# Optimization experiments

Measured on AMD Instinct MI355X. Metric: run time of the kernel, lower is better.

Reference implementation:

```python
import jax, jax.numpy as jnp
import numpy as np

B, N, D_IN, D_OUT = 512, 64, 2048, 1024
EPS = 1e-12  # layer_norm_epsilon


def setup_inputs() -> dict:
    key = jax.random.key(0)
    k0, k1, k2, k3, k4 = jax.random.split(key, 5)
    img_feats = jax.random.normal(k0, (B, N, D_IN), jnp.float32)
    boxes = jax.random.normal(k1, (B, N, 7), jnp.float32)
    box_mask = jax.random.randint(k2, (B, N), 0, 2, jnp.int32)
    obj_labels = jax.random.randint(k3, (B, N), 0, 91, jnp.int32)
    # Learned params: obj_downsample Linear(2048->1024), LayerNorm(1024)
    W = jax.random.normal(k4, (D_IN, D_OUT), jnp.float32) * 0.02
    b = jnp.zeros((D_OUT,), jnp.float32)
    ln_w = jnp.ones((D_OUT,), jnp.float32)
    ln_b = jnp.zeros((D_OUT,), jnp.float32)
    return {"img_feats": img_feats, "boxes": boxes, "box_mask": box_mask,
            "obj_labels": obj_labels, "W": W, "b": b, "ln_w": ln_w, "ln_b": ln_b}


def reference(img_feats, boxes, box_mask, obj_labels, W, b, ln_w, ln_b):
    # Dropout(p=0.1) is identity in eval mode.
    # Linear + ReLU applied to every (padded) box; per-row ops so padded rows
    # are computed then masked — same math as gathering valid rows first.
    h = jax.nn.relu(jnp.einsum('bnd,df->bnf', img_feats, W) + b)  # [B,N,1024]
    mu = jnp.mean(h, axis=-1, keepdims=True)
    var = jnp.mean(jnp.square(h - mu), axis=-1, keepdims=True)
    ln = (h - mu) * jax.lax.rsqrt(var + EPS) * ln_w + ln_b  # LayerNorm
    # pad_sequence repack: left-align each image's valid boxes (stable sort
    # keeps original order among valid boxes), zero the padded tail.
    order = jnp.argsort(1 - box_mask, axis=1, stable=True)  # valid first
    packed = jnp.take_along_axis(ln, order[:, :, None], axis=1)
    m = jnp.take_along_axis(box_mask, order, axis=1).astype(ln.dtype)
    return packed * m[:, :, None]  # obj_reps: [B, N, 1024]
```

## Files before the change

### kernel.cpp

```cpp
#include <hip/hip_runtime.h>
#include <hip/hip_bf16.h>

typedef __attribute__((ext_vector_type(8))) short short8;
typedef __attribute__((ext_vector_type(4))) short short4v;
typedef __attribute__((ext_vector_type(4))) float f32x4;

#define D_IN   2048
#define D_OUT  1024

__device__ __forceinline__ short f2bf(float x) {
    union { __hip_bfloat16 h; short s; } u;
    u.h = __float2bfloat16(x);
    return u.s;
}

__global__ void transpose_w_kernel(const float* __restrict__ W,
                                   short* __restrict__ Bt) {
    __shared__ float tile[32][33];
    int c0 = blockIdx.x * 32;
    int r0 = blockIdx.y * 32;
    int tc = threadIdx.x & 31;
    int tr = threadIdx.x >> 5;
#pragma unroll
    for (int i = 0; i < 32; i += 8)
        tile[tr + i][tc] = W[(long)(r0 + tr + i) * D_OUT + c0 + tc];
    __syncthreads();
#pragma unroll
    for (int i = 0; i < 32; i += 8)
        Bt[(long)(c0 + tr + i) * D_IN + r0 + tc] = f2bf(tile[tc][tr + i]);
}


#define BAR()    __builtin_amdgcn_s_barrier()
#define SB0()    __builtin_amdgcn_sched_barrier(0)
#define LGKM0()  do { asm volatile("s_waitcnt lgkmcnt(0)" ::: "memory"); SB0(); } while (0)

__global__ __launch_bounds__(512, 2)
void fused_kernel(const float* __restrict__ img, const short* __restrict__ Bt,
                  const float* __restrict__ bias, const int* __restrict__ mask,
                  const float* __restrict__ lnw, const float* __restrict__ lnb,
                  float* __restrict__ out) {
    __shared__ char LDS[69632];

    const int b    = blockIdx.x;
    const int tid  = threadIdx.x;
    const int lane = tid & 63;
    const int w    = tid >> 6;
    const int lrow = lane & 15;
    const int lchk = lane >> 4;

    const int brow = tid >> 2;
    const int bchk = tid & 3;
    const int bswz = bchk ^ (brow & 3) ^ ((tid >> 4) & 3);
    const short* bsrc = Bt + (long)brow * D_IN + bchk * 8;
    char* bdst = LDS + brow * 64 + bswz * 16;
    const int arl   = tid >> 3;
    const long arowg = (long)b * 64 + arl;
    const int ak4   = (tid & 7) * 4;
    const int achk  = (tid & 7) >> 1;
    char* adst = LDS + 65536 + arl * 64
               + ((achk ^ (arl & 3) ^ ((arl >> 2) & 3)) * 16) + (tid & 1) * 8;
    const int fsw = ((lchk ^ (lrow & 3) ^ ((lrow >> 2) & 3)) << 4);
    const char* afb = LDS + 65536 + lrow * 64 + fsw;
    const char* bfb = LDS + w * 8192 + lrow * 64 + fsw;

    f32x4 acc[4][8];
#pragma unroll
    for (int i = 0; i < 4; ++i)
#pragma unroll
        for (int j = 0; j < 8; ++j) acc[i][j] = (f32x4)0.0f;

    short8 bst[8];
    float4 stA;
    short8 fa[4], fb[8];

    stA = *(const float4*)(img + arowg * D_IN + ak4);
#pragma unroll
    for (int j = 0; j < 8; ++j)
        bst[j] = *(const short8*)(bsrc + (long)j * 128 * D_IN);

#pragma unroll 1
    for (int t = 0; t < 64; ++t) {
        BAR(); SB0();
        {
            short4v ca;
            ca[0] = f2bf(stA.x); ca[1] = f2bf(stA.y);
            ca[2] = f2bf(stA.z); ca[3] = f2bf(stA.w);
            *(short4v*)adst = ca;
        }
#pragma unroll
        for (int j = 0; j < 8; ++j)
            *(short8*)(bdst + j * 8192) = bst[j];
        {
            int k1 = ((t + 1) & 63) * 32;
            stA = *(const float4*)(img + arowg * D_IN + k1 + ak4);
#pragma unroll
            for (int j = 0; j < 8; ++j)
                bst[j] = *(const short8*)(bsrc + (long)j * 128 * D_IN + k1);
        }
        LGKM0();
        BAR(); SB0();
#pragma unroll
        for (int mi = 0; mi < 4; ++mi)
            fa[mi] = *(const short8*)(afb + mi * 1024);
#pragma unroll
        for (int nf = 0; nf < 8; ++nf)
            fb[nf] = *(const short8*)(bfb + nf * 1024);
        __builtin_amdgcn_s_setprio(1);
#pragma unroll
        for (int mi = 0; mi < 4; ++mi)
#pragma unroll
            for (int nf = 0; nf < 8; ++nf)
                acc[mi][nf] = __builtin_amdgcn_mfma_f32_16x16x32_bf16(
                    fa[mi], fb[nf], acc[mi][nf], 0, 0, 0);
        __builtin_amdgcn_s_setprio(0);
    }

    __syncthreads();

    float* redS = (float*)LDS;
    float* redQ = (float*)(LDS + 2048);
    float* muT  = (float*)(LDS + 4096);
    float* rsT  = (float*)(LDS + 4352);

    float bb[8];
#pragma unroll
    for (int nf = 0; nf < 8; ++nf) bb[nf] = bias[w * 128 + nf * 16 + lrow];

    float s[4][4], q[4][4];
#pragma unroll
    for (int mi = 0; mi < 4; ++mi)
#pragma unroll
        for (int r = 0; r < 4; ++r) { s[mi][r] = 0.f; q[mi][r] = 0.f; }
#pragma unroll
    for (int mi = 0; mi < 4; ++mi)
#pragma unroll
        for (int nf = 0; nf < 8; ++nf)
#pragma unroll
            for (int r = 0; r < 4; ++r) {
                float v = fmaxf(acc[mi][nf][r] + bb[nf], 0.f);
                acc[mi][nf][r] = v;
                s[mi][r] += v;
                q[mi][r] += v * v;
            }
#pragma unroll
    for (int mi = 0; mi < 4; ++mi)
#pragma unroll
        for (int r = 0; r < 4; ++r)
#pragma unroll
            for (int off = 1; off <= 8; off <<= 1) {
                s[mi][r] += __shfl_xor(s[mi][r], off);
                q[mi][r] += __shfl_xor(q[mi][r], off);
            }
    if (lrow == 0) {
#pragma unroll
        for (int mi = 0; mi < 4; ++mi)
#pragma unroll
            for (int r = 0; r < 4; ++r) {
                int m = mi * 16 + lchk * 4 + r;
                redS[w * 64 + m] = s[mi][r];
                redQ[w * 64 + m] = q[mi][r];
            }
    }
    __syncthreads();
    if (tid < 64) {
        float S = 0.f, Q = 0.f;
#pragma unroll
        for (int ww = 0; ww < 8; ++ww) { S += redS[ww * 64 + tid]; Q += redQ[ww * 64 + tid]; }
        float mu  = S * (1.0f / 1024.0f);
        float var = Q * (1.0f / 1024.0f) - mu * mu;
        muT[tid] = mu;
        rsT[tid] = rsqrtf(var + 1e-12f);
    }
    __syncthreads();

    int mv = mask[(b << 6) | lane];
    unsigned long long bal = __ballot(mv != 0);
    int cnt = __popcll(bal);

    float lw[8], lb[8];
#pragma unroll
    for (int nf = 0; nf < 8; ++nf) {
        int col = w * 128 + nf * 16 + lrow;
        lw[nf] = lnw[col];
        lb[nf] = lnb[col];
    }
#pragma unroll
    for (int mi = 0; mi < 4; ++mi)
#pragma unroll
        for (int r = 0; r < 4; ++r) {
            int m = mi * 16 + lchk * 4 + r;
            if ((bal >> m) & 1ull) {
                int d = __popcll(bal & ((1ull << m) - 1ull));
                float mu = muT[m], rs = rsT[m];
                long obase = ((long)(b << 6) + d) * D_OUT + w * 128 + lrow;
#pragma unroll
                for (int nf = 0; nf < 8; ++nf)
                    out[obase + nf * 16] = (acc[mi][nf][r] - mu) * rs * lw[nf] + lb[nf];
            }
        }
    for (int d = cnt; d < 64; ++d) {
        float2 z = make_float2(0.f, 0.f);
        *(float2*)(out + ((long)(b << 6) + d) * D_OUT + w * 128 + lane * 2) = z;
    }
}

extern "C" void kernel_launch(void* const* d_in, const int* in_sizes, int n_in,
                              void* d_out, int out_size, void* d_ws, size_t ws_size,
                              hipStream_t stream) {
    const float* img  = (const float*)d_in[0];
    const int*   mask = (const int*)d_in[2];
    const float* W    = (const float*)d_in[4];
    const float* bias = (const float*)d_in[5];
    const float* lnw  = (const float*)d_in[6];
    const float* lnb  = (const float*)d_in[7];
    float* out = (float*)d_out;

    short* Bt = (short*)d_ws;

    transpose_w_kernel<<<dim3(D_OUT / 32, D_IN / 32), 256, 0, stream>>>(W, Bt);
    fused_kernel<<<512, 512, 0, stream>>>(img, Bt, bias, mask, lnw, lnb, out);
}
```

Measured before the change: 281.3 us.

## Load B fragments directly from global into registers, bypassing LDS staging

The weight tile is no longer staged through shared memory. Each wave loads its MFMA B fragments straight from the transposed bf16 weight buffer into registers, double-buffered across two k-steps with the loop unrolled by two. LDS shrinks to 8 KB for the A tile only. This removes the B LDS writes, the B LDS reads and much of the LDS footprint. In exchange, every wave issues uncached-pattern global loads per k-step and relies on L2 for reuse, and register pressure rises from the extra fragment buffer.

```diff
diff --git a/kernel.cpp b/kernel.cpp
--- a/kernel.cpp
+++ b/kernel.cpp
@@ -40,7 +40,7 @@
                   const float* __restrict__ bias, const int* __restrict__ mask,
                   const float* __restrict__ lnw, const float* __restrict__ lnb,
                   float* __restrict__ out) {
-    __shared__ char LDS[69632];
+    __shared__ char LDS[8192];
 
     const int b    = blockIdx.x;
     const int tid  = threadIdx.x;
@@ -49,20 +49,16 @@
     const int lrow = lane & 15;
     const int lchk = lane >> 4;
 
-    const int brow = tid >> 2;
-    const int bchk = tid & 3;
-    const int bswz = bchk ^ (brow & 3) ^ ((tid >> 4) & 3);
-    const short* bsrc = Bt + (long)brow * D_IN + bchk * 8;
-    char* bdst = LDS + brow * 64 + bswz * 16;
     const int arl   = tid >> 3;
     const long arowg = (long)b * 64 + arl;
     const int ak4   = (tid & 7) * 4;
     const int achk  = (tid & 7) >> 1;
-    char* adst = LDS + 65536 + arl * 64
+    char* adst = LDS + arl * 64
                + ((achk ^ (arl & 3) ^ ((arl >> 2) & 3)) * 16) + (tid & 1) * 8;
     const int fsw = ((lchk ^ (lrow & 3) ^ ((lrow >> 2) & 3)) << 4);
-    const char* afb = LDS + 65536 + lrow * 64 + fsw;
-    const char* bfb = LDS + w * 8192 + lrow * 64 + fsw;
+    const char* afb = LDS + lrow * 64 + fsw;
+
+    const short* bsrc = Bt + (long)(w * 128 + lrow) * D_IN + lchk * 8;
 
     f32x4 acc[4][8];
 #pragma unroll
@@ -70,50 +66,55 @@
 #pragma unroll
         for (int j = 0; j < 8; ++j) acc[i][j] = (f32x4)0.0f;
 
-    short8 bst[8];
     float4 stA;
-    short8 fa[4], fb[8];
+    short8 bA[8], bB[8], fa[4];
+
+#define A_WRITE() do {                                                          \
+    short4v ca;                                                                 \
+    ca[0] = f2bf(stA.x); ca[1] = f2bf(stA.y);                                   \
+    ca[2] = f2bf(stA.z); ca[3] = f2bf(stA.w);                                   \
+    *(short4v*)adst = ca;                                                       \
+} while (0)
+#define FA_READ() do {                                                          \
+    _Pragma("unroll") for (int mi = 0; mi < 4; ++mi)                            \
+        fa[mi] = *(const short8*)(afb + mi * 1024);                             \
+} while (0)
+#define B_LOAD(dst, kt) do {                                                    \
+    _Pragma("unroll") for (int nf = 0; nf < 8; ++nf)                            \
+        dst[nf] = *(const short8*)(bsrc + (long)nf * 16 * D_IN + (kt) * 32);    \
+} while (0)
+#define MFMA_T(fb) do {                                                         \
+    __builtin_amdgcn_s_setprio(1);                                              \
+    _Pragma("unroll") for (int mi = 0; mi < 4; ++mi)                            \
+    _Pragma("unroll") for (int nf = 0; nf < 8; ++nf)                            \
+        acc[mi][nf] = __builtin_amdgcn_mfma_f32_16x16x32_bf16(                  \
+            fa[mi], fb[nf], acc[mi][nf], 0, 0, 0);                              \
+    __builtin_amdgcn_s_setprio(0);                                              \
+} while (0)
 
     stA = *(const float4*)(img + arowg * D_IN + ak4);
-#pragma unroll
-    for (int j = 0; j < 8; ++j)
-        bst[j] = *(const short8*)(bsrc + (long)j * 128 * D_IN);
+    B_LOAD(bA, 0);
 
 #pragma unroll 1
-    for (int t = 0; t < 64; ++t) {
+    for (int t = 0; t < 64; t += 2) {
         BAR(); SB0();
+        A_WRITE();
+        stA = *(const float4*)(img + arowg * D_IN + (t + 1) * 32 + ak4);
+        LGKM0(); BAR(); SB0();
+        FA_READ();
+        B_LOAD(bB, t + 1);
+        MFMA_T(bA);
+
+        BAR(); SB0();
+        A_WRITE();
         {
-            short4v ca;
-            ca[0] = f2bf(stA.x); ca[1] = f2bf(stA.y);
-            ca[2] = f2bf(stA.z); ca[3] = f2bf(stA.w);
-            *(short4v*)adst = ca;
+            int k2 = ((t + 2) & 63) * 32;
+            stA = *(const float4*)(img + arowg * D_IN + k2 + ak4);
         }
-#pragma unroll
-        for (int j = 0; j < 8; ++j)
-            *(short8*)(bdst + j * 8192) = bst[j];
-        {
-            int k1 = ((t + 1) & 63) * 32;
-            stA = *(const float4*)(img + arowg * D_IN + k1 + ak4);
-#pragma unroll
-            for (int j = 0; j < 8; ++j)
-                bst[j] = *(const short8*)(bsrc + (long)j * 128 * D_IN + k1);
-        }
-        LGKM0();
-        BAR(); SB0();
-#pragma unroll
-        for (int mi = 0; mi < 4; ++mi)
-            fa[mi] = *(const short8*)(afb + mi * 1024);
-#pragma unroll
-        for (int nf = 0; nf < 8; ++nf)
-            fb[nf] = *(const short8*)(bfb + nf * 1024);
-        __builtin_amdgcn_s_setprio(1);
-#pragma unroll
-        for (int mi = 0; mi < 4; ++mi)
-#pragma unroll
-            for (int nf = 0; nf < 8; ++nf)
-                acc[mi][nf] = __builtin_amdgcn_mfma_f32_16x16x32_bf16(
-                    fa[mi], fb[nf], acc[mi][nf], 0, 0, 0);
-        __builtin_amdgcn_s_setprio(0);
+        LGKM0(); BAR(); SB0();
+        FA_READ();
+        B_LOAD(bA, (t + 2) & 63);
+        MFMA_T(bB);
     }
 
     __syncthreads();
```

Result: slower. 316.9 us (+12.7%).
